# Kernel optimization log

Hardware: AMD Instinct MI355X
Metric: run time of the kernel (lower is better)

## Reference

```python
import jax, jax.numpy as jnp
import numpy as np

CAPACITY_FACTOR = 1.0


def setup_inputs() -> dict:
    key = jax.random.key(0)
    k1, k2, k3, k4 = jax.random.split(key, 4)
    B, T, D, E, F = 4, 2048, 2048, 8, 8192
    hidden_states = jax.random.normal(k1, (B, T, D), dtype=jnp.float32)
    w_gate = jax.random.normal(k2, (D, E), dtype=jnp.float32) * 0.02
    w1 = jax.random.normal(k3, (E, D, F), dtype=jnp.float32) * 0.02
    w2 = jax.random.normal(k4, (E, F, D), dtype=jnp.float32) * 0.02
    return {"hidden_states": hidden_states, "w_gate": w_gate, "w1": w1, "w2": w2}


def _top1_gate(x, w_gate):
    # x: [S, D]; deepspeed top1gating (no noise, no rts, drop_tokens=True)
    S, E = x.shape[0], w_gate.shape[1]
    capacity = int(CAPACITY_FACTOR * S / E)
    logits = x @ w_gate                      # [S, E]
    gates = jax.nn.softmax(logits, axis=-1)  # [S, E]
    idx1 = jnp.argmax(gates, axis=-1)        # [S]
    mask1 = jax.nn.one_hot(idx1, E, dtype=gates.dtype)          # [S, E]
    locations1 = jnp.cumsum(mask1, axis=0) - mask1              # position within expert
    mask1 = mask1 * (locations1 < capacity)                     # drop over-capacity tokens
    locations1_s = jnp.sum(locations1 * mask1, axis=1).astype(jnp.int32)  # [S]
    gates_masked = gates * mask1                                # [S, E]
    loc_oh = jax.nn.one_hot(locations1_s, capacity, dtype=gates.dtype) * jnp.sum(mask1, axis=1, keepdims=True)
    combine_weights = jnp.einsum('se,sc->sec', gates_masked, loc_oh)      # [S, E, C]
    dispatch_mask = (combine_weights > 0).astype(gates.dtype)             # [S, E, C]
    return combine_weights, dispatch_mask


def reference(hidden_states, w_gate, w1, w2):
    B, T, D = hidden_states.shape
    x = hidden_states.reshape(-1, D)                     # [S, D]
    combine_weights, dispatch_mask = _top1_gate(x, w_gate)
    # dense dispatch: [S,E,C] x [S,D] -> [E,C,D]
    dispatched = jnp.einsum('sec,sm->ecm', dispatch_mask, x)
    # per-expert FFN (GELU MLP), batched over experts
    h = jax.nn.gelu(jnp.einsum('ecd,edf->ecf', dispatched, w1))
    expert_out = jnp.einsum('ecf,efd->ecd', h, w2)       # [E, C, D]
    # dense combine: [S,E,C] x [E,C,D] -> [S,D]
    combined = jnp.einsum('sec,ecm->sm', combine_weights, expert_out)
    return combined.reshape(B, T, D)
```

## Files before the change

### kernel.cpp

```cpp
#include <hip/hip_runtime.h>

using u16 = unsigned short;
typedef __attribute__((ext_vector_type(4))) float f32x4;
typedef __attribute__((ext_vector_type(8))) short bf16x8;
typedef unsigned short u16x8 __attribute__((ext_vector_type(8)));

static constexpr int S_TOK = 8192;
static constexpr int NE    = 8;
static constexpr int CAP   = 1024;
static constexpr int DDIM  = 2048;
static constexpr int FDIM  = 8192;

#define S_WAIT_ALL() asm volatile("s_waitcnt vmcnt(0) lgkmcnt(0)" ::: "memory")
#define S_BAR()                                  \
  do {                                           \
    __builtin_amdgcn_sched_barrier(0);           \
    __builtin_amdgcn_s_barrier();                \
    __builtin_amdgcn_sched_barrier(0);           \
  } while (0)

__device__ __forceinline__ u16 f2bf(float f) {
  union { float fv; unsigned uv; } v; v.fv = f;
  unsigned r = v.uv + 0x7fffu + ((v.uv >> 16) & 1u);
  return (u16)(r >> 16);
}

__device__ __forceinline__ unsigned cvt_pk_bf16(float lo, float hi) {
  unsigned r;
  asm("v_cvt_pk_bf16_f32 %0, %1, %2" : "=v"(r) : "v"(lo), "v"(hi));
  return r;
}

__device__ __forceinline__ float gelu_tanh(float x) {
  float u = 0.7978845608028654f * (x + 0.044715f * x * x * x);
  float t = 1.0f - 2.0f / (__expf(2.0f * u) + 1.0f);
  return 0.5f * x * (1.0f + t);
}

__device__ __forceinline__ void gl_lds16(const void* g, void* l) {
  __builtin_amdgcn_global_load_lds(
      (const __attribute__((address_space(1))) unsigned int*)g,
      (__attribute__((address_space(3))) unsigned int*)l, 16, 0, 0);
}

__global__ __launch_bounds__(256) void fill_zero_kernel(float4* __restrict__ p, int n4) {
  int i = blockIdx.x * 256 + threadIdx.x;
  int stride = gridDim.x * 256;
  float4 z = {0.f, 0.f, 0.f, 0.f};
  for (; i < n4; i += stride) p[i] = z;
}

__global__ __launch_bounds__(256) void gating_kernel(
    const float* __restrict__ x, const float* __restrict__ wg,
    int* __restrict__ tok_expert, float* __restrict__ tok_gate) {
  int s = blockIdx.x * 4 + (threadIdx.x >> 6);
  int lane = threadIdx.x & 63;
  const float4* xv = (const float4*)(x + (size_t)s * DDIM + lane * 32);
  float acc[8];
#pragma unroll
  for (int e = 0; e < 8; ++e) acc[e] = 0.f;
#pragma unroll
  for (int j = 0; j < 8; ++j) {
    float4 xx = xv[j];
#pragma unroll
    for (int c = 0; c < 4; ++c) {
      int i = lane * 32 + j * 4 + c;
      const float4* wrow = (const float4*)(wg + (size_t)i * 8);
      float4 w0 = wrow[0], w1 = wrow[1];
      float xe = (c == 0) ? xx.x : (c == 1) ? xx.y : (c == 2) ? xx.z : xx.w;
      acc[0] += xe * w0.x; acc[1] += xe * w0.y; acc[2] += xe * w0.z; acc[3] += xe * w0.w;
      acc[4] += xe * w1.x; acc[5] += xe * w1.y; acc[6] += xe * w1.z; acc[7] += xe * w1.w;
    }
  }
#pragma unroll
  for (int off = 32; off > 0; off >>= 1)
#pragma unroll
    for (int e = 0; e < 8; ++e) acc[e] += __shfl_xor(acc[e], off, 64);
  if (lane == 0) {
    float m = acc[0]; int ai = 0;
#pragma unroll
    for (int e = 1; e < 8; ++e) if (acc[e] > m) { m = acc[e]; ai = e; }
    float sum = 0.f;
#pragma unroll
    for (int e = 0; e < 8; ++e) sum += expf(acc[e] - m);
    tok_expert[s] = ai;
    tok_gate[s] = 1.0f / sum;
  }
}

__global__ void init_slots(int* tok_of_slot, float* gate_of_slot) {
  int i = blockIdx.x * 256 + threadIdx.x;
  tok_of_slot[i] = -1;
  gate_of_slot[i] = 0.f;
}

__global__ __launch_bounds__(1024) void scan_kernel(
    const int* __restrict__ tok_expert, const float* __restrict__ tok_gate,
    int* __restrict__ tok_of_slot, float* __restrict__ gate_of_slot) {
  __shared__ int cnt[1024][8];
  int t = threadIdx.x;
  int e8[8];
  int local[8];
#pragma unroll
  for (int e = 0; e < 8; ++e) local[e] = 0;
#pragma unroll
  for (int j = 0; j < 8; ++j) {
    int e = tok_expert[t * 8 + j];
    e8[j] = e;
    local[e]++;
  }
#pragma unroll
  for (int e = 0; e < 8; ++e) cnt[t][e] = local[e];
  __syncthreads();
  for (int off = 1; off < 1024; off <<= 1) {
    int v[8];
    bool has = (t >= off);
    if (has) {
#pragma unroll
      for (int e = 0; e < 8; ++e) v[e] = cnt[t - off][e];
    }
    __syncthreads();
    if (has) {
#pragma unroll
      for (int e = 0; e < 8; ++e) cnt[t][e] += v[e];
    }
    __syncthreads();
  }
  int base[8];
#pragma unroll
  for (int e = 0; e < 8; ++e) base[e] = (t == 0) ? 0 : cnt[t - 1][e];
#pragma unroll
  for (int j = 0; j < 8; ++j) {
    int s = t * 8 + j;
    int e = e8[j];
    int p = base[e]++;
    if (p < CAP) {
      tok_of_slot[e * CAP + p] = s;
      gate_of_slot[e * CAP + p] = tok_gate[s];
    }
  }
}

__global__ __launch_bounds__(256) void scatter_kernel(
    const int* __restrict__ tok_of_slot, const float* __restrict__ x,
    u16* __restrict__ Xd) {
  int slot = blockIdx.x;
  int s = tok_of_slot[slot];
  int t = threadIdx.x;
  u16x8 v;
  if (s >= 0) {
    const float4* xr = (const float4*)(x + (size_t)s * DDIM + t * 8);
    float4 a = xr[0], b = xr[1];
    v[0] = f2bf(a.x); v[1] = f2bf(a.y); v[2] = f2bf(a.z); v[3] = f2bf(a.w);
    v[4] = f2bf(b.x); v[5] = f2bf(b.y); v[6] = f2bf(b.z); v[7] = f2bf(b.w);
  } else {
#pragma unroll
    for (int j = 0; j < 8; ++j) v[j] = 0;
  }
  *(u16x8*)(Xd + (size_t)slot * DDIM + t * 8) = v;
}

template <int KDIM, int NDIM, int EPI, int NEXP>
__global__ __launch_bounds__(512, 2) void moe_gemm(
    const u16* __restrict__ A, const float* __restrict__ Bf,
    u16* __restrict__ Hout, float* __restrict__ Fout,
    const int* __restrict__ tok_of_slot, const float* __restrict__ gate_of_slot,
    int e_base) {
  constexpr int MDIM = 1024;
  constexpr int BM = 256, BN = 256, BK = 64;
  constexpr int MT = MDIM / BM;
  constexpr int NK = KDIM / BK;
  constexpr int ASZ = BM * BK;
  constexpr int BSZ = BN * BK;
  constexpr int BUFSZ = ASZ + BSZ;
  __shared__ u16 lds[2 * BUFSZ];

  const int t = threadIdx.x;
  const int lane = t & 63, wave = t >> 6;
  const int wr = wave >> 2, wc = wave & 3;

  int id = blockIdx.x;
  int ez = id & (NEXP - 1);
  int w = id / NEXP;
  int mt = w & (MT - 1);
  int nt = w / MT;
  int m0 = mt * BM, n0 = nt * BN;
  int e = e_base + ez;

  const u16* Ae = A + (size_t)ez * MDIM * KDIM;
  const float* Be = Bf + (size_t)ez * (size_t)KDIM * NDIM;

  const u16* aSrc[4];
  int ldsOffA[4];
#pragma unroll
  for (int p = 0; p < 4; ++p) {
    int c = t + p * 512;
    int row = c >> 3;
    int fr = (row ^ (row >> 2)) & 7;
    int j = (c & 7) ^ fr;
    aSrc[p] = Ae + (size_t)(m0 + row) * KDIM + j * 8;
    ldsOffA[p] = c * 8;
  }

  const int bq = (t & 63) * 4;
  const int boct = t >> 6;
  const float* bP = Be + (size_t)(boct * 8) * NDIM + n0 + bq;
  int bWOff[4];
#pragma unroll
  for (int c = 0; c < 4; ++c) {
    int row = bq + c;
    int fr = (row ^ (row >> 2)) & 7;
    bWOff[c] = ASZ + row * 64 + (boct ^ fr) * 8;
  }

  const int r = lane & 15, h = lane >> 4;
  const int Kk = h ^ (r & 7) ^ (r >> 2);
  const int pE = Kk * 8;
  const int pO = (Kk ^ 4) * 8;
  const int aBase = (wr * 128 + r) * 64;
  const int bBase = ASZ + (wc * 64 + r) * 64;

  f32x4 acc[8][4];
#pragma unroll
  for (int m = 0; m < 8; ++m)
#pragma unroll
    for (int n = 0; n < 4; ++n) acc[m][n] = f32x4{0.f, 0.f, 0.f, 0.f};

  f32x4 bv4[8];

#pragma unroll
  for (int j = 0; j < 8; ++j) bv4[j] = *(const f32x4*)(bP + (size_t)j * NDIM);
#pragma unroll
  for (int p = 0; p < 4; ++p) gl_lds16(aSrc[p], &lds[ldsOffA[p]]);
#pragma unroll
  for (int c = 0; c < 4; ++c) {
    union { u16x8 v; unsigned w[4]; } o;
#pragma unroll
    for (int j = 0; j < 4; ++j) o.w[j] = cvt_pk_bf16(bv4[2 * j][c], bv4[2 * j + 1][c]);
    *(u16x8*)(&lds[bWOff[c]]) = o.v;
  }
  S_WAIT_ALL();
  S_BAR();

  for (int kt = 0; kt < NK; ++kt) {
    const u16* sb = &lds[(kt & 1) * BUFSZ];
    u16* nb = &lds[((kt + 1) & 1) * BUFSZ];
    const bool pre = (kt + 1 < NK);
    if (pre) {
      const int ko = (kt + 1) * BK;
#pragma unroll
      for (int p = 0; p < 4; ++p) gl_lds16(aSrc[p] + ko, nb + ldsOffA[p]);
#pragma unroll
      for (int j = 0; j < 8; ++j)
        bv4[j] = *(const f32x4*)(bP + (size_t)(ko + j) * NDIM);
    }

#pragma unroll
    for (int kk = 0; kk < 2; ++kk) {
      bf16x8 af[8], bv[4];
#pragma unroll
      for (int m = 0; m < 8; ++m)
        af[m] = *(const bf16x8*)(sb + aBase + m * 1024 + (((kk ^ m) & 1) ? pO : pE));
#pragma unroll
      for (int n = 0; n < 4; ++n)
        bv[n] = *(const bf16x8*)(sb + bBase + n * 1024 + (((kk ^ n) & 1) ? pO : pE));
      __builtin_amdgcn_s_setprio(1);
#pragma unroll
      for (int m = 0; m < 8; ++m)
#pragma unroll
        for (int n = 0; n < 4; ++n)
          acc[m][n] = __builtin_amdgcn_mfma_f32_16x16x32_bf16(af[m], bv[n], acc[m][n], 0, 0, 0);
      __builtin_amdgcn_s_setprio(0);
    }

    if (pre) {
#pragma unroll
      for (int c = 0; c < 4; ++c) {
        union { u16x8 v; unsigned w[4]; } o;
#pragma unroll
        for (int j = 0; j < 4; ++j) o.w[j] = cvt_pk_bf16(bv4[2 * j][c], bv4[2 * j + 1][c]);
        *(u16x8*)(nb + bWOff[c]) = o.v;
      }
    }
    S_WAIT_ALL();
    S_BAR();
  }

  if (EPI == 0) {
    u16* Hrow = Hout + (size_t)ez * MDIM * NDIM;
#pragma unroll
    for (int m = 0; m < 8; ++m) {
#pragma unroll
      for (int rr = 0; rr < 4; ++rr) {
        int row = m0 + wr * 128 + m * 16 + (lane >> 4) * 4 + rr;
#pragma unroll
        for (int n = 0; n < 4; ++n) {
          int col = n0 + wc * 64 + n * 16 + (lane & 15);
          Hrow[(size_t)row * NDIM + col] = f2bf(gelu_tanh(acc[m][n][rr]));
        }
      }
    }
  } else {
#pragma unroll
    for (int m = 0; m < 8; ++m) {
#pragma unroll
      for (int rr = 0; rr < 4; ++rr) {
        int slot_in_e = m0 + wr * 128 + m * 16 + (lane >> 4) * 4 + rr;
        int gslot = e * CAP + slot_in_e;
        int s = tok_of_slot[gslot];
        if (s >= 0) {
          float g = gate_of_slot[gslot];
#pragma unroll
          for (int n = 0; n < 4; ++n) {
            int col = n0 + wc * 64 + n * 16 + (lane & 15);
            Fout[(size_t)s * NDIM + col] = g * acc[m][n][rr];
          }
        }
      }
    }
  }
}

extern "C" void kernel_launch(void* const* d_in, const int* in_sizes, int n_in,
                              void* d_out, int out_size, void* d_ws, size_t ws_size,
                              hipStream_t stream) {
  (void)in_sizes; (void)n_in;
  const float* x  = (const float*)d_in[0];
  const float* wg = (const float*)d_in[1];
  const float* w1 = (const float*)d_in[2];
  const float* w2 = (const float*)d_in[3];
  float* out = (float*)d_out;

  char* ws = (char*)d_ws;
  size_t off = 0;
  auto alloc = [&](size_t b) {
    off = (off + 255) & ~(size_t)255;
    char* p = ws + off;
    off += b;
    return p;
  };
  int*   tok_expert   = (int*)alloc((size_t)S_TOK * 4);
  float* tok_gate     = (float*)alloc((size_t)S_TOK * 4);
  int*   tok_of_slot  = (int*)alloc((size_t)NE * CAP * 4);
  float* gate_of_slot = (float*)alloc((size_t)NE * CAP * 4);
  u16*   Xd           = (u16*)alloc((size_t)NE * CAP * DDIM * 2);
  size_t off_common = off;

  const size_t H_big = (size_t)NE * CAP * FDIM * 2;
  const size_t H_sm  = (size_t)CAP * FDIM * 2;
  bool big = ws_size >= off_common + H_big + 1024;

  fill_zero_kernel<<<2048, 256, 0, stream>>>((float4*)out, out_size / 4);
  gating_kernel<<<S_TOK / 4, 256, 0, stream>>>(x, wg, tok_expert, tok_gate);
  init_slots<<<(NE * CAP) / 256, 256, 0, stream>>>(tok_of_slot, gate_of_slot);
  scan_kernel<<<1, 1024, 0, stream>>>(tok_expert, tok_gate, tok_of_slot, gate_of_slot);
  scatter_kernel<<<NE * CAP, 256, 0, stream>>>(tok_of_slot, x, Xd);

  if (big) {
    u16* H = (u16*)alloc(H_big);
    moe_gemm<DDIM, FDIM, 0, NE><<<dim3(NE * 4 * (FDIM / 256)), 512, 0, stream>>>(
        Xd, w1, H, nullptr, tok_of_slot, gate_of_slot, 0);
    moe_gemm<FDIM, DDIM, 1, NE><<<dim3(NE * 4 * (DDIM / 256)), 512, 0, stream>>>(
        H, w2, nullptr, out, tok_of_slot, gate_of_slot, 0);
  } else {
    u16* H = (u16*)alloc(H_sm);
    for (int e = 0; e < NE; ++e) {
      moe_gemm<DDIM, FDIM, 0, 1><<<dim3(4 * (FDIM / 256)), 512, 0, stream>>>(
          Xd + (size_t)e * CAP * DDIM, w1 + (size_t)e * DDIM * FDIM, H, nullptr,
          tok_of_slot, gate_of_slot, e);
      moe_gemm<FDIM, DDIM, 1, 1><<<dim3(4 * (DDIM / 256)), 512, 0, stream>>>(
          H, w2 + (size_t)e * FDIM * DDIM, nullptr, out,
          tok_of_slot, gate_of_slot, e);
    }
  }
}
```

Measured before the change: 717.0 us.

## Deepen GEMM pipeline to prefetch two K-tiles ahead with triple-buffered A

The MoE GEMM mainloop now issues global loads two K-steps ahead. A tiles go into a triple-buffered LDS ring and B tiles alternate between two register sets, with partial vmcnt waits replacing the full wait at each barrier. This hides more global-memory latency behind the MFMA work. In exchange it uses more LDS (3 A + 2 B buffers) and more registers, so launch bounds drop to one block per SIMD pair, which lowers occupancy.

```diff
diff --git a/kernel.cpp b/kernel.cpp
--- a/kernel.cpp
+++ b/kernel.cpp
@@ -11,12 +11,16 @@
 static constexpr int DDIM  = 2048;
 static constexpr int FDIM  = 8192;
 
-#define S_WAIT_ALL() asm volatile("s_waitcnt vmcnt(0) lgkmcnt(0)" ::: "memory")
+#define SCHED0() __builtin_amdgcn_sched_barrier(0)
+#define S_VMCNT(n) do { asm volatile("s_waitcnt vmcnt(" #n ")" ::: "memory"); \
+                        SCHED0(); } while (0)
+#define LGKM0()    do { asm volatile("s_waitcnt lgkmcnt(0)" ::: "memory");    \
+                        SCHED0(); } while (0)
 #define S_BAR()                                  \
   do {                                           \
-    __builtin_amdgcn_sched_barrier(0);           \
+    SCHED0();                                    \
     __builtin_amdgcn_s_barrier();                \
-    __builtin_amdgcn_sched_barrier(0);           \
+    SCHED0();                                    \
   } while (0)
 
 __device__ __forceinline__ u16 f2bf(float f) {
@@ -161,7 +165,7 @@
 }
 
 template <int KDIM, int NDIM, int EPI, int NEXP>
-__global__ __launch_bounds__(512, 2) void moe_gemm(
+__global__ __launch_bounds__(512, 1) void moe_gemm(
     const u16* __restrict__ A, const float* __restrict__ Bf,
     u16* __restrict__ Hout, float* __restrict__ Fout,
     const int* __restrict__ tok_of_slot, const float* __restrict__ gate_of_slot,
@@ -172,8 +176,10 @@
   constexpr int NK = KDIM / BK;
   constexpr int ASZ = BM * BK;
   constexpr int BSZ = BN * BK;
-  constexpr int BUFSZ = ASZ + BSZ;
-  __shared__ u16 lds[2 * BUFSZ];
+  __shared__ u16 lds[3 * ASZ + 2 * BSZ];
+
+  u16* const Ab = lds;
+  u16* const Bb = lds + 3 * ASZ;
 
   const int t = threadIdx.x;
   const int lane = t & 63, wave = t >> 6;
@@ -210,7 +216,7 @@
   for (int c = 0; c < 4; ++c) {
     int row = bq + c;
     int fr = (row ^ (row >> 2)) & 7;
-    bWOff[c] = ASZ + row * 64 + (boct ^ fr) * 8;
+    bWOff[c] = row * 64 + (boct ^ fr) * 8;
   }
 
   const int r = lane & 15, h = lane >> 4;
@@ -218,7 +224,7 @@
   const int pE = Kk * 8;
   const int pO = (Kk ^ 4) * 8;
   const int aBase = (wr * 128 + r) * 64;
-  const int bBase = ASZ + (wc * 64 + r) * 64;
+  const int bBase = (wc * 64 + r) * 64;
 
   f32x4 acc[8][4];
 #pragma unroll
@@ -226,33 +232,54 @@
 #pragma unroll
     for (int n = 0; n < 4; ++n) acc[m][n] = f32x4{0.f, 0.f, 0.f, 0.f};
 
-  f32x4 bv4[8];
-
-#pragma unroll
-  for (int j = 0; j < 8; ++j) bv4[j] = *(const f32x4*)(bP + (size_t)j * NDIM);
-#pragma unroll
-  for (int p = 0; p < 4; ++p) gl_lds16(aSrc[p], &lds[ldsOffA[p]]);
+  f32x4 bvE[8], bvO[8];
+
+#pragma unroll
+  for (int j = 0; j < 8; ++j) bvE[j] = *(const f32x4*)(bP + (size_t)j * NDIM);
+  SCHED0();
+#pragma unroll
+  for (int p = 0; p < 4; ++p) gl_lds16(aSrc[p], Ab + ldsOffA[p]);
+  SCHED0();
+#pragma unroll
+  for (int j = 0; j < 8; ++j) bvO[j] = *(const f32x4*)(bP + (size_t)(BK + j) * NDIM);
+  SCHED0();
+#pragma unroll
+  for (int p = 0; p < 4; ++p) gl_lds16(aSrc[p] + BK, Ab + ASZ + ldsOffA[p]);
+  SCHED0();
+  S_VMCNT(16);
 #pragma unroll
   for (int c = 0; c < 4; ++c) {
     union { u16x8 v; unsigned w[4]; } o;
 #pragma unroll
-    for (int j = 0; j < 4; ++j) o.w[j] = cvt_pk_bf16(bv4[2 * j][c], bv4[2 * j + 1][c]);
-    *(u16x8*)(&lds[bWOff[c]]) = o.v;
-  }
-  S_WAIT_ALL();
+    for (int j = 0; j < 4; ++j) o.w[j] = cvt_pk_bf16(bvE[2 * j][c], bvE[2 * j + 1][c]);
+    *(u16x8*)(Bb + bWOff[c]) = o.v;
+  }
+  S_VMCNT(12);
+  LGKM0();
   S_BAR();
 
+  int aC = 0;
   for (int kt = 0; kt < NK; ++kt) {
-    const u16* sb = &lds[(kt & 1) * BUFSZ];
-    u16* nb = &lds[((kt + 1) & 1) * BUFSZ];
-    const bool pre = (kt + 1 < NK);
-    if (pre) {
-      const int ko = (kt + 1) * BK;
-#pragma unroll
-      for (int p = 0; p < 4; ++p) gl_lds16(aSrc[p] + ko, nb + ldsOffA[p]);
-#pragma unroll
-      for (int j = 0; j < 8; ++j)
-        bv4[j] = *(const f32x4*)(bP + (size_t)(ko + j) * NDIM);
+    const u16* sa = Ab + aC * ASZ;
+    const u16* sbB = Bb + (kt & 1) * BSZ;
+    u16* nbB = Bb + ((kt + 1) & 1) * BSZ;
+    int a2 = aC + 2; if (a2 >= 3) a2 -= 3;
+    const bool pre2 = (kt + 2 < NK);
+    const bool pre1 = (kt + 1 < NK);
+
+    if (pre2) {
+      const int ko = (kt + 2) * BK;
+      if ((kt & 1) == 0) {
+#pragma unroll
+        for (int j = 0; j < 8; ++j) bvE[j] = *(const f32x4*)(bP + (size_t)(ko + j) * NDIM);
+      } else {
+#pragma unroll
+        for (int j = 0; j < 8; ++j) bvO[j] = *(const f32x4*)(bP + (size_t)(ko + j) * NDIM);
+      }
+      SCHED0();
+#pragma unroll
+      for (int p = 0; p < 4; ++p) gl_lds16(aSrc[p] + ko, Ab + a2 * ASZ + ldsOffA[p]);
+      SCHED0();
     }
 
 #pragma unroll
@@ -260,10 +287,10 @@
       bf16x8 af[8], bv[4];
 #pragma unroll
       for (int m = 0; m < 8; ++m)
-        af[m] = *(const bf16x8*)(sb + aBase + m * 1024 + (((kk ^ m) & 1) ? pO : pE));
+        af[m] = *(const bf16x8*)(sa + aBase + m * 1024 + (((kk ^ m) & 1) ? pO : pE));
 #pragma unroll
       for (int n = 0; n < 4; ++n)
-        bv[n] = *(const bf16x8*)(sb + bBase + n * 1024 + (((kk ^ n) & 1) ? pO : pE));
+        bv[n] = *(const bf16x8*)(sbB + bBase + n * 1024 + (((kk ^ n) & 1) ? pO : pE));
       __builtin_amdgcn_s_setprio(1);
 #pragma unroll
       for (int m = 0; m < 8; ++m)
@@ -273,17 +300,30 @@
       __builtin_amdgcn_s_setprio(0);
     }
 
-    if (pre) {
-#pragma unroll
-      for (int c = 0; c < 4; ++c) {
-        union { u16x8 v; unsigned w[4]; } o;
-#pragma unroll
-        for (int j = 0; j < 4; ++j) o.w[j] = cvt_pk_bf16(bv4[2 * j][c], bv4[2 * j + 1][c]);
-        *(u16x8*)(nb + bWOff[c]) = o.v;
+    if (pre1) {
+      if (pre2) { S_VMCNT(12); }
+      else      { S_VMCNT(0); }
+      if ((kt & 1) == 0) {
+#pragma unroll
+        for (int c = 0; c < 4; ++c) {
+          union { u16x8 v; unsigned w[4]; } o;
+#pragma unroll
+          for (int j = 0; j < 4; ++j) o.w[j] = cvt_pk_bf16(bvO[2 * j][c], bvO[2 * j + 1][c]);
+          *(u16x8*)(nbB + bWOff[c]) = o.v;
+        }
+      } else {
+#pragma unroll
+        for (int c = 0; c < 4; ++c) {
+          union { u16x8 v; unsigned w[4]; } o;
+#pragma unroll
+          for (int j = 0; j < 4; ++j) o.w[j] = cvt_pk_bf16(bvE[2 * j][c], bvE[2 * j + 1][c]);
+          *(u16x8*)(nbB + bWOff[c]) = o.v;
+        }
       }
-    }
-    S_WAIT_ALL();
+      LGKM0();
+    }
     S_BAR();
+    aC = (aC + 1 == 3) ? 0 : aC + 1;
   }
 
   if (EPI == 0) {
@@ -292,10 +332,10 @@
     for (int m = 0; m < 8; ++m) {
 #pragma unroll
       for (int rr = 0; rr < 4; ++rr) {
-        int row = m0 + wr * 128 + m * 16 + (lane >> 4) * 4 + rr;
+        int row = m0 + wr * 128 + m * 16 + h * 4 + rr;
 #pragma unroll
         for (int n = 0; n < 4; ++n) {
-          int col = n0 + wc * 64 + n * 16 + (lane & 15);
+          int col = n0 + wc * 64 + n * 16 + r;
           Hrow[(size_t)row * NDIM + col] = f2bf(gelu_tanh(acc[m][n][rr]));
         }
       }
@@ -305,14 +345,14 @@
     for (int m = 0; m < 8; ++m) {
 #pragma unroll
       for (int rr = 0; rr < 4; ++rr) {
-        int slot_in_e = m0 + wr * 128 + m * 16 + (lane >> 4) * 4 + rr;
+        int slot_in_e = m0 + wr * 128 + m * 16 + h * 4 + rr;
         int gslot = e * CAP + slot_in_e;
         int s = tok_of_slot[gslot];
         if (s >= 0) {
           float g = gate_of_slot[gslot];
 #pragma unroll
           for (int n = 0; n < 4; ++n) {
-            int col = n0 + wc * 64 + n * 16 + (lane & 15);
+            int col = n0 + wc * 64 + n * 16 + r;
             Fout[(size_t)s * NDIM + col] = g * acc[m][n][rr];
           }
         }
```

Result: slower. 1.268 ms (+76.8%).
